# Optimization experiments

Measured on AMD Instinct MI355X. Metric: run time of the kernel, lower is better.

The kernel has to match this reference:

```python
import jax, jax.numpy as jnp
import numpy as np

B, S, HID = 1, 2048, 4096
H, HKV, DFULL, D = 32, 8, 128, 96
GROUPS = H // HKV
SCALE = DFULL ** -0.5  # scaling uses the FULL head_dim per the source
ROPE_THETA = 10000.0


def setup_inputs() -> dict:
    key = jax.random.key(0)
    ks = jax.random.split(key, 8)
    hidden_states = jax.random.normal(ks[0], (B, S, HID), jnp.float32)
    # standard HF Llama RoPE tables over the FULL head dim
    inv_freq = 1.0 / (ROPE_THETA ** (jnp.arange(0, DFULL, 2, dtype=jnp.float32) / DFULL))
    ang = jnp.arange(S, dtype=jnp.float32)[:, None] * inv_freq[None, :]  # [S, DFULL/2]
    emb = jnp.concatenate([ang, ang], axis=-1)  # [S, DFULL]
    cos = jnp.cos(emb)[None]  # [1, S, DFULL]
    sin = jnp.sin(emb)[None]
    # per-kv-head frequency indices: lo half in [0, DFULL/2), hi half = lo + DFULL/2
    half, dh = DFULL // 2, D // 2
    idx_lo = jax.random.randint(ks[1], (HKV, dh), 0, half)
    indices = jnp.concatenate([idx_lo, idx_lo + half], axis=-1).astype(jnp.int32)  # [HKV, D]
    s = 0.02
    Wq = jax.random.normal(ks[2], (H * D, HID), jnp.float32) * s
    Wk = jax.random.normal(ks[3], (HKV * D, HID), jnp.float32) * s
    Wv = jax.random.normal(ks[4], (HKV * D, HID), jnp.float32) * s
    Wo = jax.random.normal(ks[5], (HID, H * D), jnp.float32) * s
    return {"hidden_states": hidden_states, "cos": cos, "sin": sin,
            "indices": indices, "Wq": Wq, "Wk": Wk, "Wv": Wv, "Wo": Wo}


def rotate_half(x):
    x1, x2 = jnp.split(x, 2, axis=-1)
    return jnp.concatenate([-x2, x1], axis=-1)


def reference(hidden_states, cos, sin, indices, Wq, Wk, Wv, Wo):
    b, s, _ = hidden_states.shape
    # QKV projections (no bias), reshape to [B, heads, S, D]
    q = (hidden_states @ Wq.T).reshape(b, s, H, D).transpose(0, 2, 1, 3)
    k = (hidden_states @ Wk.T).reshape(b, s, HKV, D).transpose(0, 2, 1, 3)
    v = (hidden_states @ Wv.T).reshape(b, s, HKV, D).transpose(0, 2, 1, 3)
    # indexed RoPE: gather per-kv-head frequencies from the full-dim tables
    cos_h = cos[:, :, indices].transpose(0, 2, 1, 3)  # [B, HKV, S, D]
    sin_h = sin[:, :, indices].transpose(0, 2, 1, 3)
    cos_q = jnp.repeat(cos_h, GROUPS, axis=1)  # [B, H, S, D]
    sin_q = jnp.repeat(sin_h, GROUPS, axis=1)
    q = q * cos_q + rotate_half(q) * sin_q
    k = k * cos_h + rotate_half(k) * sin_h
    # GQA: repeat kv to num_attention_heads
    k = jnp.repeat(k, GROUPS, axis=1)  # [B, H, S, D]
    v = jnp.repeat(v, GROUPS, axis=1)
    scores = jnp.einsum('bhqd,bhkd->bhqk', q, k) * SCALE
    causal = jnp.tril(jnp.ones((s, s), dtype=bool))
    scores = jnp.where(causal[None, None], scores, jnp.finfo(scores.dtype).min)
    probs = jax.nn.softmax(scores, axis=-1)
    out = jnp.einsum('bhqk,bhkd->bhqd', probs, v)  # [B, H, S, D]
    out = out.transpose(0, 2, 1, 3).reshape(b, s, H * D)
    return out @ Wo.T
```

## Files before the change

kernel.cpp:

```cpp
#include <hip/hip_runtime.h>

typedef unsigned short u16;
typedef unsigned int u32;
typedef __bf16 bf16x8 __attribute__((ext_vector_type(8)));
typedef float f32x4 __attribute__((ext_vector_type(4)));

#define SCALE_Q2 0.12751743443398106f

#define GLDS16(gp, lp)                                                        \
  __builtin_amdgcn_global_load_lds(                                           \
      (const __attribute__((address_space(1))) void*)(gp),                    \
      (__attribute__((address_space(3))) void*)(lp), 16, 0, 0)

__device__ __forceinline__ u16 f2bf(float f) {
  u32 u = __builtin_bit_cast(u32, f);
  u += 0x7fffu + ((u >> 16) & 1u);
  return (u16)(u >> 16);
}
__device__ __forceinline__ float bf2f(u16 b) {
  u32 u = ((u32)b) << 16;
  return __builtin_bit_cast(float, u);
}

__global__ __launch_bounds__(256) void cvt_kernel(const float* __restrict__ src,
                                                  u16* __restrict__ dst, int n4) {
  int i = blockIdx.x * 256 + threadIdx.x;
  if (i >= n4) return;
  float4 v = ((const float4*)src)[i];
  u32 lo = (u32)f2bf(v.x) | ((u32)f2bf(v.y) << 16);
  u32 hi = (u32)f2bf(v.z) | ((u32)f2bf(v.w) << 16);
  ((uint2*)dst)[i] = make_uint2(lo, hi);
}

template <int NREP, bool BF16OUT>
__global__ __launch_bounds__(512, 2) void gemm8p(const u16* __restrict__ A,
                                                 const u16* __restrict__ B,
                                                 void* __restrict__ Cout,
                                                 int M, int N, int K) {
  constexpr int BN = NREP * 64;
  __shared__ u16 As[2 * 256 * 64];
  __shared__ u16 Bs[2 * BN * 64];
  const int tid = threadIdx.x;
  const int w = tid >> 6, lane = tid & 63, quad = lane >> 4, c16 = lane & 15;

  const int nx = gridDim.x;
  const int orig = blockIdx.y * nx + blockIdx.x;
  const int nwg = nx * gridDim.y;
  const int id = (orig & 7) * (nwg >> 3) + (orig >> 3);
  const int n0 = (id % nx) * BN, m0 = (id / nx) * 256;

  const int wm = (w & 1) * 128, wn = (w >> 1) * (NREP * 16);
  const int srow8 = lane >> 3, scg = (lane & 7) ^ srow8;
  const u16* Ag = A + (size_t)(m0 + w * 8 + srow8) * K + scg * 8;
  const u16* Bg = B + (size_t)(n0 + w * 8 + srow8) * K + scg * 8;
  const int axor = c16 & 7;

  f32x4 acc[8][NREP];
#pragma unroll
  for (int i = 0; i < 8; ++i)
#pragma unroll
    for (int j = 0; j < NREP; ++j) acc[i][j] = (f32x4){0.f, 0.f, 0.f, 0.f};

  const int NT = K >> 6;

#pragma unroll
  for (int j = 0; j < 4; ++j)
    GLDS16(Ag + (size_t)(j * 64) * K, &As[(j * 64 + w * 8) * 64]);
#pragma unroll
  for (int j = 0; j < NREP; ++j)
    GLDS16(Bg + (size_t)(j * 64) * K, &Bs[(j * 64 + w * 8) * 64]);

  for (int t = 0; t < NT; ++t) {
    const int sl = t & 1;
    const u16* as = &As[sl * (256 * 64)];
    const u16* bs = &Bs[sl * (BN * 64)];
    u16* asn = &As[(sl ^ 1) * (256 * 64)];
    u16* bsn = &Bs[(sl ^ 1) * (BN * 64)];
    const int kn = (t + 1) * 64;
    const bool pf = (t + 1 < NT);

    if (pf) {
#pragma unroll
      for (int j = 0; j < 4; ++j)
        GLDS16(Ag + (size_t)(j * 64) * K + kn, &asn[(j * 64 + w * 8) * 64]);
      asm volatile("s_waitcnt vmcnt(4)" ::: "memory");
    } else {
      asm volatile("s_waitcnt vmcnt(0)" ::: "memory");
    }
    __builtin_amdgcn_s_barrier();
    asm volatile("" ::: "memory");

    bf16x8 bfr[NREP][2];
#pragma unroll
    for (int nt = 0; nt < NREP; ++nt)
#pragma unroll
      for (int kk = 0; kk < 2; ++kk)
        bfr[nt][kk] = *(const bf16x8*)&bs[(wn + nt * 16 + c16) * 64 +
                                          (((kk * 4 + quad) ^ axor) * 8)];

#pragma unroll
    for (int ph = 0; ph < 4; ++ph) {
      bf16x8 afr[2][2];
#pragma unroll
      for (int i = 0; i < 2; ++i)
#pragma unroll
        for (int kk = 0; kk < 2; ++kk)
          afr[i][kk] = *(const bf16x8*)&as[(wm + (ph * 2 + i) * 16 + c16) * 64 +
                                            (((kk * 4 + quad) ^ axor) * 8)];
      if (ph == 1 && pf) {
#pragma unroll
        for (int j = 0; j < NREP; ++j)
          GLDS16(Bg + (size_t)(j * 64) * K + kn, &bsn[(j * 64 + w * 8) * 64]);
      }
      __builtin_amdgcn_s_setprio(1);
#pragma unroll
      for (int i = 0; i < 2; ++i)
#pragma unroll
        for (int nt = 0; nt < NREP; ++nt)
#pragma unroll
          for (int kk = 0; kk < 2; ++kk)
            acc[ph * 2 + i][nt] = __builtin_amdgcn_mfma_f32_16x16x32_bf16(
                afr[i][kk], bfr[nt][kk], acc[ph * 2 + i][nt], 0, 0, 0);
      __builtin_amdgcn_s_setprio(0);
    }
    asm volatile("" ::: "memory");
    __builtin_amdgcn_s_barrier();
  }

#pragma unroll
  for (int mt = 0; mt < 8; ++mt)
#pragma unroll
    for (int nt = 0; nt < NREP; ++nt)
#pragma unroll
      for (int r = 0; r < 4; ++r) {
        int m = m0 + wm + mt * 16 + quad * 4 + r;
        int n = n0 + wn + nt * 16 + c16;
        if (BF16OUT)
          ((u16*)Cout)[(size_t)m * N + n] = f2bf(acc[mt][nt][r]);
        else
          ((float*)Cout)[(size_t)m * N + n] = acc[mt][nt][r];
      }
}

__global__ __launch_bounds__(256) void rope_kernel(const u16* __restrict__ qkv,
                                                   const float* __restrict__ cosb,
                                                   const float* __restrict__ sinb,
                                                   const int* __restrict__ idxs,
                                                   u16* __restrict__ qB,
                                                   u16* __restrict__ kB) {
  u32 i = blockIdx.x * 256u + threadIdx.x;
  const u32 NQ = 2048u * 32u * 96u;
  if (i < NQ) {
    u32 s = i / 3072u, rem = i % 3072u;
    u32 h = rem / 96u, d = rem % 96u;
    u32 hkv = h >> 2;
    u32 base = s * 4608u + h * 96u + d;
    float x = bf2f(qkv[base]);
    float pv = (d < 48u) ? -bf2f(qkv[base + 48u]) : bf2f(qkv[base - 48u]);
    int idx = idxs[hkv * 96u + d];
    float c = cosb[s * 128u + idx], sn = sinb[s * 128u + idx];
    qB[(h * 2048u + s) * 96u + d] = f2bf((x * c + pv * sn) * SCALE_Q2);
  } else {
    u32 j = i - NQ;
    u32 s = j / 768u, rem = j % 768u;
    u32 hkv = rem / 96u, d = rem % 96u;
    u32 base = s * 4608u + 3072u + hkv * 96u + d;
    float x = bf2f(qkv[base]);
    float pv = (d < 48u) ? -bf2f(qkv[base + 48u]) : bf2f(qkv[base - 48u]);
    int idx = idxs[hkv * 96u + d];
    float c = cosb[s * 128u + idx], sn = sinb[s * 128u + idx];
    kB[(hkv * 2048u + s) * 96u + d] = f2bf(x * c + pv * sn);
  }
}

__global__ __launch_bounds__(256) void vtrans_kernel(const u16* __restrict__ qkvB,
                                                     u16* __restrict__ vtB) {
  __shared__ u16 T[64 * 34];
  const int s0 = blockIdx.x * 64, d0 = blockIdx.y * 32;
  const int tx = threadIdx.x & 31, ty = threadIdx.x >> 5;
#pragma unroll
  for (int it = 0; it < 8; it++) {
    int row = it * 8 + ty;
    T[row * 34 + tx] = qkvB[(size_t)(s0 + row) * 4608 + 3840 + d0 + tx];
  }
  __syncthreads();
  const int sx = threadIdx.x & 63, dy = threadIdx.x >> 6;
#pragma unroll
  for (int it = 0; it < 8; it++) {
    int d = it * 4 + dy;
    vtB[(size_t)(d0 + d) * 2048 + s0 + sx] = T[sx * 34 + d];
  }
}

__global__ __launch_bounds__(256) void attn_kernel(const u16* __restrict__ qB,
                                                   const u16* __restrict__ kB,
                                                   const u16* __restrict__ vtB,
                                                   u16* __restrict__ aoB) {
  __shared__ u16 Ks[64 * 96];
  __shared__ u16 Vs[96 * 64];
  __shared__ u16 Ps[4 * 16 * 64];
  const int tid = threadIdx.x;
  const int w = tid >> 6, lane = tid & 63, quad = lane >> 4, c16 = lane & 15;
  const int pr = blockIdx.x, h = blockIdx.y, hkv = h >> 2;
  u16* pw = Ps + w * (16 * 64);

  size_t voff[3];
#pragma unroll
  for (int it = 0; it < 3; it++) {
    int j = it * 256 + tid;
    int row = j >> 3, c = (j & 7) ^ (row & 7);
    voff[it] = (size_t)row * 2048 + c * 8;
  }
  const u16* kbase = kB + (size_t)hkv * 2048 * 96;
  const u16* vbase = vtB + (size_t)hkv * 96 * 2048;

  bf16x8 vones;
#pragma unroll
  for (int i = 0; i < 8; i++) vones[i] = (__bf16)1.0f;

  for (int ph = 0; ph < 2; ph++) {
    const int qt = ph ? (31 - pr) : pr;
    const int m_base = qt * 64 + w * 16;

    bf16x8 qf[3];
    {
      const u16* qrow = qB + ((size_t)h * 2048 + m_base + c16) * 96;
#pragma unroll
      for (int t = 0; t < 3; t++) qf[t] = *(const bf16x8*)(qrow + t * 32 + quad * 8);
    }
    f32x4 o[6], ol;
#pragma unroll
    for (int dt = 0; dt < 6; dt++) o[dt] = (f32x4){0.f, 0.f, 0.f, 0.f};
    ol = (f32x4){0.f, 0.f, 0.f, 0.f};

    for (int kt = 0; kt <= qt; kt++) {
      const int k0 = kt * 64;
      __syncthreads();
#pragma unroll
      for (int it = 0; it < 3; it++) {
        GLDS16(kbase + (size_t)k0 * 96 + (it * 256 + tid) * 8,
               &Ks[(it * 256 + w * 64) * 8]);
        GLDS16(vbase + voff[it] + k0, &Vs[(it * 256 + w * 64) * 8]);
      }
      __syncthreads();

      f32x4 sacc[4];
#pragma unroll
      for (int nt = 0; nt < 4; nt++) sacc[nt] = (f32x4){0.f, 0.f, 0.f, 0.f};
#pragma unroll
      for (int nt = 0; nt < 4; nt++)
#pragma unroll
        for (int t = 0; t < 3; t++) {
          bf16x8 kf = *(const bf16x8*)(&Ks[(nt * 16 + c16) * 96 + t * 32 + quad * 8]);
          sacc[nt] = __builtin_amdgcn_mfma_f32_16x16x32_bf16(qf[t], kf, sacc[nt], 0, 0, 0);
        }

      if (kt == qt) {
#pragma unroll
        for (int r = 0; r < 4; r++) {
          int row_abs = m_base + quad * 4 + r;
#pragma unroll
          for (int nt = 0; nt < 4; nt++)
            if (k0 + nt * 16 + c16 > row_abs) sacc[nt][r] = -__builtin_inff();
        }
      }

#pragma unroll
      for (int r = 0; r < 4; r++) {
        int mrow = quad * 4 + r, m7 = mrow & 7;
#pragma unroll
        for (int nt = 0; nt < 4; nt++) {
          float p = __builtin_amdgcn_exp2f(sacc[nt][r]);
          int chunk = (nt * 2 + (c16 >> 3)) ^ m7;
          pw[mrow * 64 + chunk * 8 + (c16 & 7)] =
              (u16)(__builtin_bit_cast(u32, p) >> 16);
        }
      }
      bf16x8 pf[2];
#pragma unroll
      for (int kti = 0; kti < 2; kti++) {
        int chunk = (kti * 4 + quad) ^ (c16 & 7);
        pf[kti] = *(const bf16x8*)(&pw[c16 * 64 + chunk * 8]);
      }
#pragma unroll
      for (int kti = 0; kti < 2; kti++) {
        ol = __builtin_amdgcn_mfma_f32_16x16x32_bf16(pf[kti], vones, ol, 0, 0, 0);
#pragma unroll
        for (int dt = 0; dt < 6; dt++) {
          int row = dt * 16 + c16;
          int vch = (kti * 4 + quad) ^ (row & 7);
          bf16x8 vf = *(const bf16x8*)(&Vs[row * 64 + vch * 8]);
          o[dt] = __builtin_amdgcn_mfma_f32_16x16x32_bf16(pf[kti], vf, o[dt], 0, 0, 0);
        }
      }
    }

#pragma unroll
    for (int r = 0; r < 4; r++) {
      float inv = 1.0f / ol[r];
      int row = m_base + quad * 4 + r;
#pragma unroll
      for (int dt = 0; dt < 6; dt++)
        aoB[(size_t)row * 3072 + h * 96 + dt * 16 + c16] = f2bf(o[dt][r] * inv);
    }
  }
}

extern "C" void kernel_launch(void* const* d_in, const int* in_sizes, int n_in,
                              void* d_out, int out_size, void* d_ws, size_t ws_size,
                              hipStream_t stream) {
  const float* hs   = (const float*)d_in[0];
  const float* cosb = (const float*)d_in[1];
  const float* sinb = (const float*)d_in[2];
  const int*   idxs = (const int*)d_in[3];
  const float* Wq   = (const float*)d_in[4];
  const float* Wk   = (const float*)d_in[5];
  const float* Wv   = (const float*)d_in[6];
  const float* Wo   = (const float*)d_in[7];
  float* out = (float*)d_out;
  char* ws = (char*)d_ws;

  u16* hsB   = (u16*)(ws);
  u16* wqkvB = (u16*)(ws + 16777216);
  u16* woB   = (u16*)(ws + 54525952);
  u16* qkvB  = (u16*)(ws + 79691776);
  u16* qB    = (u16*)(ws + 98566144);
  u16* kB    = (u16*)(ws + 111149056);
  u16* vtB   = (u16*)(ws + 114294784);
  u16* aoB   = (u16*)(ws + 117440512);

  cvt_kernel<<<8192, 256, 0, stream>>>(hs, hsB, 2097152);
  cvt_kernel<<<12288, 256, 0, stream>>>(Wq, wqkvB, 3145728);
  cvt_kernel<<<3072, 256, 0, stream>>>(Wk, wqkvB + 3072 * 4096, 786432);
  cvt_kernel<<<3072, 256, 0, stream>>>(Wv, wqkvB + 3840 * 4096, 786432);
  cvt_kernel<<<12288, 256, 0, stream>>>(Wo, woB, 3145728);

  gemm8p<3, true><<<dim3(24, 8), 512, 0, stream>>>(hsB, wqkvB, qkvB, 2048, 4608, 4096);

  rope_kernel<<<30720, 256, 0, stream>>>(qkvB, cosb, sinb, idxs, qB, kB);
  vtrans_kernel<<<dim3(32, 24), 256, 0, stream>>>(qkvB, vtB);

  attn_kernel<<<dim3(16, 32), 256, 0, stream>>>(qB, kB, vtB, aoB);

  gemm8p<2, false><<<dim3(32, 8), 512, 0, stream>>>(aoB, woB, out, 2048, 4096, 3072);
}
```

Measured before the change: 439.5 us.

## Interleave GEMM tile prefetch across MFMA phases with fine-grained vmcnt waits

Result: slower. 557.5 us (+26.8%).

```diff
diff --git a/kernel.cpp b/kernel.cpp
--- a/kernel.cpp
+++ b/kernel.cpp
@@ -11,6 +11,27 @@
   __builtin_amdgcn_global_load_lds(                                           \
       (const __attribute__((address_space(1))) void*)(gp),                    \
       (__attribute__((address_space(3))) void*)(lp), 16, 0, 0)
+
+#define BARRIER()                                                             \
+  do {                                                                        \
+    asm volatile("" ::: "memory");                                            \
+    __builtin_amdgcn_s_barrier();                                             \
+    asm volatile("" ::: "memory");                                            \
+  } while (0)
+
+#define LGKM0()                                                               \
+  do {                                                                        \
+    asm volatile("s_waitcnt lgkmcnt(0)" ::: "memory");                        \
+    __builtin_amdgcn_sched_barrier(0);                                        \
+  } while (0)
+
+template <int N>
+__device__ __forceinline__ void vmwait() {
+  if constexpr (N == 0) asm volatile("s_waitcnt vmcnt(0)" ::: "memory");
+  else if constexpr (N == 2) asm volatile("s_waitcnt vmcnt(2)" ::: "memory");
+  else if constexpr (N == 4) asm volatile("s_waitcnt vmcnt(4)" ::: "memory");
+  else if constexpr (N == 5) asm volatile("s_waitcnt vmcnt(5)" ::: "memory");
+}
 
 __device__ __forceinline__ u16 f2bf(float f) {
   u32 u = __builtin_bit_cast(u32, f);
@@ -63,68 +84,83 @@
 
   const int NT = K >> 6;
 
-#pragma unroll
-  for (int j = 0; j < 4; ++j)
-    GLDS16(Ag + (size_t)(j * 64) * K, &As[(j * 64 + w * 8) * 64]);
-#pragma unroll
-  for (int j = 0; j < NREP; ++j)
-    GLDS16(Bg + (size_t)(j * 64) * K, &Bs[(j * 64 + w * 8) * 64]);
+  {
+    u16* ab = &As[0];
+    u16* bb = &Bs[0];
+#pragma unroll
+    for (int j = 0; j < NREP; ++j)
+      GLDS16(Bg + (size_t)(j * 64) * K, &bb[(j * 64 + w * 8) * 64]);
+    GLDS16(Ag + (size_t)(0 * 64) * K, &ab[(0 * 64 + w * 8) * 64]);
+    GLDS16(Ag + (size_t)(2 * 64) * K, &ab[(2 * 64 + w * 8) * 64]);
+    GLDS16(Ag + (size_t)(1 * 64) * K, &ab[(1 * 64 + w * 8) * 64]);
+    GLDS16(Ag + (size_t)(3 * 64) * K, &ab[(3 * 64 + w * 8) * 64]);
+  }
+  vmwait<2>();
+  BARRIER();
 
   for (int t = 0; t < NT; ++t) {
-    const int sl = t & 1;
-    const u16* as = &As[sl * (256 * 64)];
-    const u16* bs = &Bs[sl * (BN * 64)];
-    u16* asn = &As[(sl ^ 1) * (256 * 64)];
-    u16* bsn = &Bs[(sl ^ 1) * (BN * 64)];
+    const u16* as = &As[(t & 1) * (256 * 64)];
+    const u16* bs = &Bs[(t & 1) * (BN * 64)];
+    u16* asn = &As[((t + 1) & 1) * (256 * 64)];
+    u16* bsn = &Bs[((t + 1) & 1) * (BN * 64)];
     const int kn = (t + 1) * 64;
     const bool pf = (t + 1 < NT);
 
-    if (pf) {
-#pragma unroll
-      for (int j = 0; j < 4; ++j)
-        GLDS16(Ag + (size_t)(j * 64) * K + kn, &asn[(j * 64 + w * 8) * 64]);
-      asm volatile("s_waitcnt vmcnt(4)" ::: "memory");
-    } else {
-      asm volatile("s_waitcnt vmcnt(0)" ::: "memory");
-    }
-    __builtin_amdgcn_s_barrier();
-    asm volatile("" ::: "memory");
-
     bf16x8 bfr[NREP][2];
-#pragma unroll
-    for (int nt = 0; nt < NREP; ++nt)
-#pragma unroll
-      for (int kk = 0; kk < 2; ++kk)
-        bfr[nt][kk] = *(const bf16x8*)&bs[(wn + nt * 16 + c16) * 64 +
-                                          (((kk * 4 + quad) ^ axor) * 8)];
 
 #pragma unroll
     for (int ph = 0; ph < 4; ++ph) {
-      bf16x8 afr[2][2];
-#pragma unroll
-      for (int i = 0; i < 2; ++i)
-#pragma unroll
-        for (int kk = 0; kk < 2; ++kk)
-          afr[i][kk] = *(const bf16x8*)&as[(wm + (ph * 2 + i) * 16 + c16) * 64 +
-                                            (((kk * 4 + quad) ^ axor) * 8)];
-      if (ph == 1 && pf) {
+      if (ph == 0 && pf) {
 #pragma unroll
         for (int j = 0; j < NREP; ++j)
           GLDS16(Bg + (size_t)(j * 64) * K + kn, &bsn[(j * 64 + w * 8) * 64]);
       }
+      if (ph == 1 && pf) {
+        GLDS16(Ag + (size_t)(0 * 64) * K + kn, &asn[(0 * 64 + w * 8) * 64]);
+        GLDS16(Ag + (size_t)(2 * 64) * K + kn, &asn[(2 * 64 + w * 8) * 64]);
+      }
+      if (ph == 2 && pf) {
+        GLDS16(Ag + (size_t)(1 * 64) * K + kn, &asn[(1 * 64 + w * 8) * 64]);
+        GLDS16(Ag + (size_t)(3 * 64) * K + kn, &asn[(3 * 64 + w * 8) * 64]);
+      }
+
+      if (ph == 0) {
+#pragma unroll
+        for (int nt = 0; nt < NREP; ++nt)
+#pragma unroll
+          for (int kk = 0; kk < 2; ++kk)
+            bfr[nt][kk] = *(const bf16x8*)&bs[(wn + nt * 16 + c16) * 64 +
+                                              (((kk * 4 + quad) ^ axor) * 8)];
+      }
+      bf16x8 af[2][2];
+#pragma unroll
+      for (int i = 0; i < 2; ++i)
+#pragma unroll
+        for (int kk = 0; kk < 2; ++kk)
+          af[i][kk] = *(const bf16x8*)&as[(wm + (ph * 2 + i) * 16 + c16) * 64 +
+                                           (((kk * 4 + quad) ^ axor) * 8)];
+
+      if (ph == 1) {
+        if (pf) vmwait<NREP + 2>();
+        else    vmwait<0>();
+      }
+      if (ph == 3 && pf) vmwait<2>();
+
+      BARRIER();
+      LGKM0();
       __builtin_amdgcn_s_setprio(1);
 #pragma unroll
-      for (int i = 0; i < 2; ++i)
-#pragma unroll
-        for (int nt = 0; nt < NREP; ++nt)
-#pragma unroll
-          for (int kk = 0; kk < 2; ++kk)
+      for (int kk = 0; kk < 2; ++kk)
+#pragma unroll
+        for (int i = 0; i < 2; ++i)
+#pragma unroll
+          for (int nt = 0; nt < NREP; ++nt)
             acc[ph * 2 + i][nt] = __builtin_amdgcn_mfma_f32_16x16x32_bf16(
-                afr[i][kk], bfr[nt][kk], acc[ph * 2 + i][nt], 0, 0, 0);
+                af[i][kk], bfr[nt][kk], acc[ph * 2 + i][nt], 0, 0, 0);
       __builtin_amdgcn_s_setprio(0);
+      __builtin_amdgcn_sched_barrier(0);
+      BARRIER();
     }
-    asm volatile("" ::: "memory");
-    __builtin_amdgcn_s_barrier();
   }
 
 #pragma unroll
```
